# Kernel optimization log

Measured on AMD Instinct MI355X. Metric: run time of the kernel, lower is better.

## Reference

```python
import jax, jax.numpy as jnp
import numpy as np

B, T, C, H, HS = 4, 2048, 1024, 16, 64
EPS = 1e-5


def setup_inputs() -> dict:
    key = jax.random.key(0)
    ks = jax.random.split(key, 16)
    s = lambda k, shp, fan: jax.random.normal(k, shp, jnp.float32) * (fan ** -0.5)
    return {
        "x": jax.random.normal(ks[0], (B, T, C), jnp.float32),
        "wq": s(ks[1], (H, C, HS), C), "bq": jnp.zeros((H, HS), jnp.float32),
        "wk": s(ks[2], (H, C, HS), C), "bk": jnp.zeros((H, HS), jnp.float32),
        "wv": s(ks[3], (H, C, HS), C), "bv": jnp.zeros((H, HS), jnp.float32),
        "wp": s(ks[4], (C, C), C), "bp": jnp.zeros((C,), jnp.float32),
        "w1": s(ks[5], (C, 4 * C), C), "b1": jnp.zeros((4 * C,), jnp.float32),
        "w2": s(ks[6], (4 * C, C), 4 * C), "b2": jnp.zeros((C,), jnp.float32),
        "g1": jnp.ones((C,), jnp.float32), "be1": jnp.zeros((C,), jnp.float32),
        "g2": jnp.ones((C,), jnp.float32), "be2": jnp.zeros((C,), jnp.float32),
    }


def _layernorm(x, g, b):
    mu = jnp.mean(x, axis=-1, keepdims=True)
    var = jnp.mean(jnp.square(x - mu), axis=-1, keepdims=True)
    return (x - mu) * jax.lax.rsqrt(var + EPS) * g + b


def reference(x, wq, bq, wk, bk, wv, bv, wp, bp, w1, b1, w2, b2, g1, be1, g2, be2):
    Bc, Tc, Cc = x.shape
    h = _layernorm(x, g1, be1)
    # per-head projections stacked: [B,H,T,HS]
    q = jnp.einsum('btc,hcd->bhtd', h, wq) + bq[None, :, None, :]
    k = jnp.einsum('btc,hcd->bhtd', h, wk) + bk[None, :, None, :]
    v = jnp.einsum('btc,hcd->bhtd', h, wv) + bv[None, :, None, :]
    # NOTE: source scales by 1/sqrt(n_embd), not 1/sqrt(head_size)
    scores = jnp.einsum('bhtd,bhsd->bhts', q, k) * (Cc ** -0.5)
    causal = jnp.tril(jnp.ones((Tc, Tc), bool))
    scores = jnp.where(causal, scores, -jnp.inf)
    attn = jax.nn.softmax(scores, axis=-1)
    out = jnp.einsum('bhts,bhsd->bhtd', attn, v)
    out = out.transpose(0, 2, 1, 3).reshape(Bc, Tc, Cc)  # concat heads
    x = x + out @ wp + bp
    h2 = _layernorm(x, g2, be2)
    ffn = jax.nn.relu(h2 @ w1 + b1) @ w2 + b2
    return x + ffn
```

## Files before the change

kernel.cpp:

```cpp
#include <hip/hip_runtime.h>


constexpr int Bb = 4, Tt = 2048, Cc = 1024, Hh = 16, HSz = 64, Ff = 4096;
constexpr int Mrows = Bb * Tt;

typedef __attribute__((ext_vector_type(8))) short bf16x8;
typedef __attribute__((ext_vector_type(4))) float f32x4;

__device__ __forceinline__ ushort f2bf(float f) {
  uint u = __builtin_bit_cast(uint, f);
  uint r = (u + 0x7fffu + ((u >> 16) & 1u)) >> 16;
  return (ushort)r;
}
__device__ __forceinline__ float bf2f(ushort s) {
  return __builtin_bit_cast(float, ((uint)s) << 16);
}
__device__ __forceinline__ uint cvtpk_bf16(float lo, float hi) {
  uint r;
  asm("v_cvt_pk_bf16_f32 %0, %1, %2" : "=v"(r) : "v"(lo), "v"(hi));
  return r;
}
__device__ __forceinline__ void gload16(const void* g, void* l) {
  __builtin_amdgcn_global_load_lds(
      (const __attribute__((address_space(1))) void*)g,
      (__attribute__((address_space(3))) void*)l, 16, 0, 0);
}
#define VMCNT0 asm volatile("s_waitcnt vmcnt(0)" ::: "memory")
#define LGKM0                                          \
  do {                                                 \
    asm volatile("s_waitcnt lgkmcnt(0)" ::: "memory"); \
    __builtin_amdgcn_sched_barrier(0);                 \
  } while (0)
#define BARRIER __builtin_amdgcn_s_barrier()

__global__ __launch_bounds__(256) void ln_kernel(const float* __restrict__ x,
                                                 const float* __restrict__ g,
                                                 const float* __restrict__ b,
                                                 ushort* __restrict__ out) {
  int row = blockIdx.x;
  const float* xr = x + (size_t)row * Cc;
  int c4 = threadIdx.x * 4;
  float4 v = *(const float4*)(xr + c4);
  float s1 = v.x + v.y + v.z + v.w;
  float s2 = v.x * v.x + v.y * v.y + v.z * v.z + v.w * v.w;
#pragma unroll
  for (int off = 32; off >= 1; off >>= 1) {
    s1 += __shfl_xor(s1, off);
    s2 += __shfl_xor(s2, off);
  }
  __shared__ float red[8];
  int wid = threadIdx.x >> 6, lane = threadIdx.x & 63;
  if (lane == 0) { red[wid] = s1; red[4 + wid] = s2; }
  __syncthreads();
  float t1 = red[0] + red[1] + red[2] + red[3];
  float t2 = red[4] + red[5] + red[6] + red[7];
  float mu = t1 * (1.0f / Cc);
  float var = t2 * (1.0f / Cc) - mu * mu;
  float rs = rsqrtf(var + 1e-5f);
  float4 gv = *(const float4*)(g + c4);
  float4 bv = *(const float4*)(b + c4);
  ushort4 o;
  o.x = f2bf((v.x - mu) * rs * gv.x + bv.x);
  o.y = f2bf((v.y - mu) * rs * gv.y + bv.y);
  o.z = f2bf((v.z - mu) * rs * gv.z + bv.z);
  o.w = f2bf((v.w - mu) * rs * gv.w + bv.w);
  *(ushort4*)(out + (size_t)row * Cc + c4) = o;
}

__device__ __forceinline__ void tcast_body(const float* __restrict__ src,
                                           ushort* __restrict__ dst, int ldS,
                                           int ldD, int r0, int c0) {
  __shared__ float t[32][33];
  int c = threadIdx.x & 31, r8 = threadIdx.x >> 5;
#pragma unroll
  for (int i = 0; i < 4; ++i) {
    int r = r8 + i * 8;
    t[r][c] = src[(size_t)(r0 + r) * ldS + c0 + c];
  }
  __syncthreads();
#pragma unroll
  for (int i = 0; i < 4; ++i) {
    int rr = r8 + i * 8;
    dst[(size_t)(c0 + rr) * ldD + r0 + c] = f2bf(t[c][rr]);
  }
}

__global__ __launch_bounds__(256) void tcast_kernel(const float* __restrict__ src,
                                                    ushort* __restrict__ dst,
                                                    int ldS, int ldD) {
  tcast_body(src, dst, ldS, ldD, blockIdx.x * 32, blockIdx.y * 32);
}

__global__ __launch_bounds__(256) void tcast_qkv(const float* __restrict__ wq,
                                                 const float* __restrict__ wk,
                                                 const float* __restrict__ wv,
                                                 ushort* __restrict__ dst) {
  int z = blockIdx.z, zz = z >> 4, h = z & 15;
  const float* src = (zz == 0 ? wq : (zz == 1 ? wk : wv)) + (size_t)h * Cc * HSz;
  ushort* d = dst + (size_t)(zz * 1024 + h * 64) * 1024;
  tcast_body(src, d, HSz, Cc, blockIdx.x * 32, blockIdx.y * 32);
}

__global__ __launch_bounds__(256) void bias_concat(const float* __restrict__ bq,
                                                   const float* __restrict__ bk,
                                                   const float* __restrict__ bv,
                                                   float* __restrict__ dst) {
  int i = blockIdx.x * 256 + threadIdx.x;
  dst[i] = i < 1024 ? bq[i] : (i < 2048 ? bk[i - 1024] : bv[i - 2048]);
}

__device__ __forceinline__ void xcd_swz(int& bx, int& by) {
  int bid = blockIdx.x + blockIdx.y * gridDim.x;
  int cpx = (gridDim.x * gridDim.y) >> 3;
  int id = (bid & 7) * cpx + (bid >> 3);
  bx = id % gridDim.x;
  by = id / gridDim.x;
}

template <int MH, int NH>
__device__ __forceinline__ void mfma16(f32x4 (&acc)[8][4], bf16x8 (&a)[4][2],
                                       bf16x8 (&b)[2][2]) {
#pragma unroll
  for (int m = 0; m < 4; ++m)
#pragma unroll
    for (int n = 0; n < 2; ++n)
#pragma unroll
      for (int kk = 0; kk < 2; ++kk)
        acc[MH * 4 + m][NH * 2 + n] = __builtin_amdgcn_mfma_f32_16x16x32_bf16(
            a[m][kk], b[n][kk], acc[MH * 4 + m][NH * 2 + n], 0, 0, 0);
}

__device__ __forceinline__ void gemm256_main(const ushort* __restrict__ A,
                                             const ushort* __restrict__ Bt,
                                             int m0, int n0,
                                             ushort* __restrict__ As,
                                             ushort* __restrict__ Bs,
                                             f32x4 (&acc)[8][4]) {
  constexpr int NKT = 16;
  int tid = threadIdx.x, wid = tid >> 6, lane = tid & 63;
  int wr = wid >> 2, wc = wid & 3, fr = lane & 15, fq = lane >> 4;
  const ushort* Ag = A + (size_t)m0 * 1024;
  const ushort* Bg = Bt + (size_t)n0 * 1024;
  int r0 = tid >> 3, r1 = 64 + (tid >> 3);
  int sc = ((tid & 7) ^ ((tid >> 3) & 7)) << 3;

  auto stage = [&](int ktn, int h, int ns) {
    const ushort* g = (h < 2) ? Ag : Bg;
    ushort* l = ((h < 2) ? As : Bs) + ns * 16384 + (h & 1) * 8192;
    int kcol = ktn * 64, rbase = (h & 1) * 128;
    gload16(g + (size_t)(rbase + r0) * 1024 + kcol + sc, l + (size_t)wid * 512);
    gload16(g + (size_t)(rbase + r1) * 1024 + kcol + sc,
            l + (size_t)(512 + wid * 64) * 8);
  };
  auto readA = [&](int slot, int mh, bf16x8 (&a)[4][2]) {
#pragma unroll
    for (int m = 0; m < 4; ++m) {
      int row = wr * 128 + mh * 64 + m * 16 + fr;
#pragma unroll
      for (int kk = 0; kk < 2; ++kk)
        a[m][kk] = *(const bf16x8*)&As[slot * 16384 + row * 64 +
                                       (((kk * 4 + fq) ^ (row & 7)) << 3)];
    }
  };
  auto readB = [&](int slot, int nh, bf16x8 (&b)[2][2]) {
#pragma unroll
    for (int n = 0; n < 2; ++n) {
      int row = wc * 64 + nh * 32 + n * 16 + fr;
#pragma unroll
      for (int kk = 0; kk < 2; ++kk)
        b[n][kk] = *(const bf16x8*)&Bs[slot * 16384 + row * 64 +
                                       (((kk * 4 + fq) ^ (row & 7)) << 3)];
    }
  };

  stage(0, 0, 0); stage(0, 1, 0); stage(0, 2, 0); stage(0, 3, 0);
  VMCNT0;
  BARRIER;

  bf16x8 a[4][2], b0[2][2], b1[2][2];
#pragma unroll 1
  for (int kt = 0; kt < NKT; ++kt) {
    int slot = kt & 1, ns = slot ^ 1;
    bool st = (kt + 1 < NKT);
    readA(slot, 0, a);
    readB(slot, 0, b0);
    if (st) { stage(kt + 1, 0, ns); stage(kt + 1, 2, ns); }
    BARRIER;
    LGKM0;
    __builtin_amdgcn_s_setprio(1);
    mfma16<0, 0>(acc, a, b0);
    __builtin_amdgcn_s_setprio(0);
    BARRIER;
    readB(slot, 1, b1);
    if (st) { stage(kt + 1, 1, ns); stage(kt + 1, 3, ns); }
    BARRIER;
    LGKM0;
    __builtin_amdgcn_s_setprio(1);
    mfma16<0, 1>(acc, a, b1);
    __builtin_amdgcn_s_setprio(0);
    BARRIER;
    readA(slot, 1, a);
    BARRIER;
    LGKM0;
    __builtin_amdgcn_s_setprio(1);
    mfma16<1, 0>(acc, a, b0);
    __builtin_amdgcn_s_setprio(0);
    BARRIER;
    __builtin_amdgcn_s_setprio(1);
    mfma16<1, 1>(acc, a, b1);
    __builtin_amdgcn_s_setprio(0);
    VMCNT0;
    BARRIER;
  }
}

__global__ __launch_bounds__(512, 2) void gemm256_relu(
    const ushort* __restrict__ A, const ushort* __restrict__ Bt,
    const float* __restrict__ bias, ushort* __restrict__ Cout, int ldc) {
  __shared__ __align__(16) ushort As[2 * 256 * 64];
  __shared__ __align__(16) ushort Bs[2 * 256 * 64];
  f32x4 acc[8][4] = {};
  int bx, by;
  xcd_swz(bx, by);
  int m0 = by * 256, n0 = bx * 256;
  gemm256_main(A, Bt, m0, n0, As, Bs, acc);
  int lane = threadIdx.x & 63, wid = threadIdx.x >> 6;
  int wr = wid >> 2, wc = wid & 3, fr = lane & 15, fq = lane >> 4;
#pragma unroll
  for (int i = 0; i < 8; ++i) {
    int gm = m0 + wr * 128 + (i >> 2) * 64 + (i & 3) * 16 + fq * 4;
#pragma unroll
    for (int j2 = 0; j2 < 4; ++j2) {
      int gn = n0 + wc * 64 + (j2 >> 1) * 32 + (j2 & 1) * 16 + fr;
      float bsv = bias[gn];
#pragma unroll
      for (int j = 0; j < 4; ++j)
        Cout[(size_t)(gm + j) * ldc + gn] = f2bf(fmaxf(acc[i][j2][j] + bsv, 0.f));
    }
  }
}

__global__ __launch_bounds__(512, 2) void gemm256_ffn2(
    const ushort* __restrict__ A, int lda, const ushort* __restrict__ Bt,
    int ldb, const float* __restrict__ bias, const float* __restrict__ res,
    float* __restrict__ Cout, int ldc, int K) {
  __shared__ __align__(16) ushort As[2 * 256 * 64];
  __shared__ __align__(16) ushort Bs[2 * 128 * 64];
  f32x4 acc[8][2] = {};
  int bx, by;
  xcd_swz(bx, by);
  int m0 = by * 256, n0 = bx * 128;
  int tid = threadIdx.x, wid = tid >> 6, lane = tid & 63;
  int wr = wid >> 2, wc = wid & 3, fr = lane & 15, fq = lane >> 4;
  const ushort* Ag = A + (size_t)m0 * lda;
  const ushort* Bg = Bt + (size_t)n0 * ldb;
  int r0 = tid >> 3, r1 = 64 + (tid >> 3);
  int sc = ((tid & 7) ^ ((tid >> 3) & 7)) << 3;
  int NKT = K >> 6;

  auto stageA = [&](int ktn, int h, int ns) {
    ushort* l = As + ns * 16384 + h * 8192;
    int kcol = ktn * 64, rbase = h * 128;
    gload16(Ag + (size_t)(rbase + r0) * lda + kcol + sc, l + (size_t)wid * 512);
    gload16(Ag + (size_t)(rbase + r1) * lda + kcol + sc,
            l + (size_t)(512 + wid * 64) * 8);
  };
  auto stageB = [&](int ktn, int h, int ns) {
    ushort* l = Bs + ns * 8192 + h * 4096;
    int kcol = ktn * 64, rbase = h * 64;
    gload16(Bg + (size_t)(rbase + r0) * ldb + kcol + sc, l + (size_t)wid * 512);
  };
  auto readA = [&](int slot, int mh, bf16x8 (&a)[4][2]) {
#pragma unroll
    for (int m = 0; m < 4; ++m) {
      int row = wr * 128 + mh * 64 + m * 16 + fr;
#pragma unroll
      for (int kk = 0; kk < 2; ++kk)
        a[m][kk] = *(const bf16x8*)&As[slot * 16384 + row * 64 +
                                       (((kk * 4 + fq) ^ (row & 7)) << 3)];
    }
  };
  auto readB = [&](int slot, int nh, bf16x8 (&b)[2]) {
    int row = wc * 32 + nh * 16 + fr;
#pragma unroll
    for (int kk = 0; kk < 2; ++kk)
      b[kk] = *(const bf16x8*)&Bs[slot * 8192 + row * 64 +
                                  (((kk * 4 + fq) ^ (row & 7)) << 3)];
  };
  auto mfma8 = [&](int mh, int nh, bf16x8 (&a)[4][2], bf16x8 (&b)[2]) {
#pragma unroll
    for (int m = 0; m < 4; ++m)
#pragma unroll
      for (int kk = 0; kk < 2; ++kk)
        acc[mh * 4 + m][nh] = __builtin_amdgcn_mfma_f32_16x16x32_bf16(
            a[m][kk], b[kk], acc[mh * 4 + m][nh], 0, 0, 0);
  };

  stageA(0, 0, 0); stageA(0, 1, 0); stageB(0, 0, 0); stageB(0, 1, 0);
  VMCNT0;
  BARRIER;

  bf16x8 a[4][2], b0[2], b1[2];
#pragma unroll 1
  for (int kt = 0; kt < NKT; ++kt) {
    int slot = kt & 1, ns = slot ^ 1;
    bool st = (kt + 1 < NKT);
    readA(slot, 0, a);
    readB(slot, 0, b0);
    if (st) { stageA(kt + 1, 0, ns); stageB(kt + 1, 0, ns); }
    BARRIER;
    LGKM0;
    __builtin_amdgcn_s_setprio(1);
    mfma8(0, 0, a, b0);
    __builtin_amdgcn_s_setprio(0);
    BARRIER;
    readB(slot, 1, b1);
    if (st) { stageA(kt + 1, 1, ns); stageB(kt + 1, 1, ns); }
    BARRIER;
    LGKM0;
    __builtin_amdgcn_s_setprio(1);
    mfma8(0, 1, a, b1);
    __builtin_amdgcn_s_setprio(0);
    BARRIER;
    readA(slot, 1, a);
    BARRIER;
    LGKM0;
    __builtin_amdgcn_s_setprio(1);
    mfma8(1, 0, a, b0);
    __builtin_amdgcn_s_setprio(0);
    BARRIER;
    __builtin_amdgcn_s_setprio(1);
    mfma8(1, 1, a, b1);
    __builtin_amdgcn_s_setprio(0);
    VMCNT0;
    BARRIER;
  }

#pragma unroll
  for (int i = 0; i < 8; ++i) {
    int gm = m0 + wr * 128 + (i >> 2) * 64 + (i & 3) * 16 + fq * 4;
#pragma unroll
    for (int nh = 0; nh < 2; ++nh) {
      int gn = n0 + wc * 32 + nh * 16 + fr;
      float bsv = bias[gn];
#pragma unroll
      for (int j = 0; j < 4; ++j) {
        int row = gm + j;
        Cout[(size_t)row * ldc + gn] =
            acc[i][nh][j] + bsv + res[(size_t)row * ldc + gn];
      }
    }
  }
}

__device__ __forceinline__ void gemm_main(const ushort* __restrict__ A, int lda,
                                          const ushort* __restrict__ Bt, int ldb,
                                          int K, int m0, int n0,
                                          ushort* __restrict__ As,
                                          ushort* __restrict__ Bs,
                                          f32x4 (&acc)[4][2]) {
  int tid = threadIdx.x, wid = tid >> 6, lane = tid & 63;
  int wr = wid >> 2, wc = wid & 3, fr = lane & 15, fq = lane >> 4;
  const ushort* Ag = A + (size_t)m0 * lda;
  const ushort* Bg = Bt + (size_t)n0 * ldb;
  for (int k0 = 0; k0 < K; k0 += 64) {
#pragma unroll
    for (int c = 0; c < 2; ++c) {
      int slot = c * 512 + tid;
      int row = slot >> 3, s = slot & 7;
      int sw = (s << 3) ^ ((row & 7) << 3);
      gload16(Ag + (size_t)row * lda + k0 + sw, As + (size_t)(c * 512 + wid * 64) * 8);
      gload16(Bg + (size_t)row * ldb + k0 + sw, Bs + (size_t)(c * 512 + wid * 64) * 8);
    }
    __syncthreads();
    bf16x8 av[4][2], bv[2][2];
#pragma unroll
    for (int m = 0; m < 4; ++m) {
      int row = wr * 64 + m * 16 + fr;
#pragma unroll
      for (int ks = 0; ks < 2; ++ks)
        av[m][ks] = *(const bf16x8*)&As[row * 64 + (((ks * 4 + fq) ^ (row & 7)) << 3)];
    }
#pragma unroll
    for (int n = 0; n < 2; ++n) {
      int row = wc * 32 + n * 16 + fr;
#pragma unroll
      for (int ks = 0; ks < 2; ++ks)
        bv[n][ks] = *(const bf16x8*)&Bs[row * 64 + (((ks * 4 + fq) ^ (row & 7)) << 3)];
    }
#pragma unroll
    for (int m = 0; m < 4; ++m)
#pragma unroll
      for (int n = 0; n < 2; ++n)
#pragma unroll
        for (int ks = 0; ks < 2; ++ks)
          acc[m][n] = __builtin_amdgcn_mfma_f32_16x16x32_bf16(
              av[m][ks], bv[n][ks], acc[m][n], 0, 0, 0);
    __syncthreads();
  }
}

template <bool RELU, bool HASRES, bool OUTBF16>
__global__ __launch_bounds__(512) void gemm_bf16(
    const ushort* __restrict__ A, int lda, const ushort* __restrict__ Bt,
    int ldb, const float* __restrict__ bias, const float* __restrict__ res,
    void* __restrict__ Cout, int ldc, int K) {
  __shared__ __align__(16) ushort As[128 * 64];
  __shared__ __align__(16) ushort Bs[128 * 64];
  f32x4 acc[4][2] = {};
  int bx, by;
  xcd_swz(bx, by);
  int m0 = by * 128, n0 = bx * 128;
  gemm_main(A, lda, Bt, ldb, K, m0, n0, As, Bs, acc);
  int lane = threadIdx.x & 63, wid = threadIdx.x >> 6;
  int wr = wid >> 2, wc = wid & 3, fr = lane & 15, fq = lane >> 4;
#pragma unroll
  for (int m = 0; m < 4; ++m) {
    int gm = m0 + wr * 64 + m * 16 + fq * 4;
#pragma unroll
    for (int n = 0; n < 2; ++n) {
      int gn = n0 + wc * 32 + n * 16 + fr;
      float bsv = bias[gn];
#pragma unroll
      for (int j = 0; j < 4; ++j) {
        int row = gm + j;
        float v = acc[m][n][j] + bsv;
        if constexpr (HASRES) v += res[(size_t)row * ldc + gn];
        if constexpr (RELU) v = fmaxf(v, 0.f);
        if constexpr (OUTBF16)
          ((ushort*)Cout)[(size_t)row * ldc + gn] = f2bf(v);
        else
          ((float*)Cout)[(size_t)row * ldc + gn] = v;
      }
    }
  }
}

__global__ __launch_bounds__(512) void gemm_qkv(const ushort* __restrict__ A,
                                                const ushort* __restrict__ Bt,
                                                const float* __restrict__ bias,
                                                ushort* __restrict__ q,
                                                ushort* __restrict__ k,
                                                ushort* __restrict__ vt) {
  __shared__ __align__(16) ushort As[128 * 64];
  __shared__ __align__(16) ushort Bs[128 * 64];
  f32x4 acc[4][2] = {};
  int bx, by;
  xcd_swz(bx, by);
  int m0 = by * 128, n0 = bx * 128;
  gemm_main(A, 1024, Bt, 1024, 1024, m0, n0, As, Bs, acc);
  int lane = threadIdx.x & 63, wid = threadIdx.x >> 6;
  int wr = wid >> 2, wc = wid & 3, fr = lane & 15, fq = lane >> 4;
  const float qscale = 1.4426950408889634f / 32.0f;
#pragma unroll
  for (int m = 0; m < 4; ++m) {
    int gm = m0 + wr * 64 + m * 16 + fq * 4;
#pragma unroll
    for (int n = 0; n < 2; ++n) {
      int gn = n0 + wc * 32 + n * 16 + fr;
      float bsv = bias[gn];
      if (gn < 1024) {
#pragma unroll
        for (int j = 0; j < 4; ++j)
          q[(size_t)(gm + j) * 1024 + gn] = f2bf((acc[m][n][j] + bsv) * qscale);
      } else if (gn < 2048) {
        int col = gn - 1024;
#pragma unroll
        for (int j = 0; j < 4; ++j)
          k[(size_t)(gm + j) * 1024 + col] = f2bf(acc[m][n][j] + bsv);
      } else {
        int dd = gn - 2048, h = dd >> 6, d = dd & 63;
        int bbr = gm >> 11, t = gm & 2047;
        ushort4 pw = {f2bf(acc[m][n][0] + bsv), f2bf(acc[m][n][1] + bsv),
                      f2bf(acc[m][n][2] + bsv), f2bf(acc[m][n][3] + bsv)};
        *(ushort4*)&vt[(((size_t)(bbr * 16 + h)) * 64 + d) * 2048 + t] = pw;
      }
    }
  }
}

constexpr int QB = 128, KVB = 64;
__global__ __launch_bounds__(512) void attn_kernel(const ushort* __restrict__ Qb,
                                                   const ushort* __restrict__ Kb,
                                                   const ushort* __restrict__ Vt,
                                                   ushort* __restrict__ att) {
  __shared__ __align__(16) ushort Klds[2][64 * 64];
  __shared__ __align__(16) ushort Vlds[2][64 * 64];
  __shared__ __align__(16) ushort Plds[8][16 * 64];
  int tid = threadIdx.x, wid = tid >> 6, lane = tid & 63;
  int fr = lane & 15, fq = lane >> 4;
  int bh = blockIdx.y, bb = bh >> 4, hh = bh & 15;
  const ushort* qkbase = Qb + ((size_t)bb * Tt) * Cc + hh * HSz;
  const ushort* Kbase = Kb + ((size_t)bb * Tt) * Cc + hh * HSz;
  const ushort* Vbase = Vt + ((size_t)(bb * Hh + hh)) * HSz * Tt;
  int srow = tid >> 3;
  int ssw = ((tid & 7) << 3) ^ ((srow & 7) << 3);

#pragma unroll 1
  for (int pass = 0; pass < 2; ++pass) {
    int qt = pass ? (Tt / QB - 1 - (int)blockIdx.x) : (int)blockIdx.x;
    int q0 = qt * QB;
    int q0w = q0 + wid * 16;

    bf16x8 Qreg[2];
#pragma unroll
    for (int d2 = 0; d2 < 2; ++d2)
      Qreg[d2] = *(const bf16x8*)(qkbase + (size_t)(q0w + fr) * Cc + d2 * 32 + fq * 8);
    f32x4 Oa[4] = {};
    float mrow = -1e30f, lrow = 0.f;
    int nt = q0 / KVB + 2;

    __syncthreads();
    gload16(Kbase + (size_t)srow * Cc + ssw, (char*)Klds[0] + wid * 1024);
    gload16(Vbase + (size_t)srow * Tt + ssw, (char*)Vlds[0] + wid * 1024);

#pragma unroll 1
    for (int kt = 0; kt < nt; ++kt) {
      int t0 = kt * KVB;
      int c = kt & 1;
      __syncthreads();
      if (kt + 1 < nt) {
        int t0n = t0 + KVB;
        gload16(Kbase + (size_t)(t0n + srow) * Cc + ssw,
                (char*)Klds[c ^ 1] + wid * 1024);
        gload16(Vbase + (size_t)srow * Tt + t0n + ssw,
                (char*)Vlds[c ^ 1] + wid * 1024);
      }
      if (q0w + 15 < t0) continue;

      const char* Kc = (const char*)Klds[c];
      const char* Vc = (const char*)Vlds[c];
      bf16x8 kf[4][2];
#pragma unroll
      for (int ks = 0; ks < 4; ++ks)
#pragma unroll
        for (int d2 = 0; d2 < 2; ++d2) {
          int row = ks * 16 + fr;
          int off = (d2 * 64 + fq * 16) ^ ((row & 7) << 4);
          kf[ks][d2] = *(const bf16x8*)(Kc + row * 128 + off);
        }
      f32x4 accs[4] = {};
      __builtin_amdgcn_s_setprio(1);
#pragma unroll
      for (int ks = 0; ks < 4; ++ks) {
        accs[ks] = __builtin_amdgcn_mfma_f32_16x16x32_bf16(
            kf[ks][0], Qreg[0], accs[ks], 0, 0, 0);
        accs[ks] = __builtin_amdgcn_mfma_f32_16x16x32_bf16(
            kf[ks][1], Qreg[1], accs[ks], 0, 0, 0);
      }
      __builtin_amdgcn_s_setprio(0);

      float sv[4][4];
      float vmax = -1e30f;
      if (t0 + 63 <= q0w) {
#pragma unroll
        for (int ks = 0; ks < 4; ++ks)
#pragma unroll
          for (int j = 0; j < 4; ++j) {
            sv[ks][j] = accs[ks][j];
            vmax = fmaxf(vmax, sv[ks][j]);
          }
      } else {
        int qg = q0w + fr;
#pragma unroll
        for (int ks = 0; ks < 4; ++ks)
#pragma unroll
          for (int j = 0; j < 4; ++j) {
            int kg = t0 + ks * 16 + fq * 4 + j;
            float s = accs[ks][j];
            s = (kg <= qg) ? s : -1e30f;
            sv[ks][j] = s;
            vmax = fmaxf(vmax, s);
          }
      }
      float mnew = mrow;
      if (!__all(vmax <= mrow + 11.0f)) {
        float rmax = fmaxf(vmax, __shfl_xor(vmax, 16));
        rmax = fmaxf(rmax, __shfl_xor(rmax, 32));
        mnew = fmaxf(mrow, rmax);
        float sf = exp2f(mrow - mnew);
        mrow = mnew;
        lrow *= sf;
#pragma unroll
        for (int j = 0; j < 4; ++j) {
          float sfo = __shfl(sf, fq * 4 + j);
#pragma unroll
          for (int ds = 0; ds < 4; ++ds) Oa[ds][j] *= sfo;
        }
      }
      char* pbase = (char*)Plds[wid] + fr * 128;
#pragma unroll
      for (int ks = 0; ks < 4; ++ks) {
        float p0 = exp2f(sv[ks][0] - mnew);
        float p1 = exp2f(sv[ks][1] - mnew);
        float p2 = exp2f(sv[ks][2] - mnew);
        float p3 = exp2f(sv[ks][3] - mnew);
        lrow += (p0 + p1) + (p2 + p3);
        uint2 pw = {cvtpk_bf16(p0, p1), cvtpk_bf16(p2, p3)};
        int off = (ks * 32 + fq * 8) ^ ((fr & 7) << 4);
        *(uint2*)(pbase + off) = pw;
      }

      bf16x8 vf[4][2];
#pragma unroll
      for (int ds = 0; ds < 4; ++ds)
#pragma unroll
        for (int k2 = 0; k2 < 2; ++k2) {
          int row = ds * 16 + fr;
          int off = (k2 * 64 + fq * 16) ^ ((row & 7) << 4);
          vf[ds][k2] = *(const bf16x8*)(Vc + row * 128 + off);
        }
      bf16x8 pf[2];
#pragma unroll
      for (int k2 = 0; k2 < 2; ++k2) {
        int off = (k2 * 64 + fq * 16) ^ ((fr & 7) << 4);
        pf[k2] = *(const bf16x8*)((const char*)Plds[wid] + fr * 128 + off);
      }
      __builtin_amdgcn_s_setprio(1);
#pragma unroll
      for (int ds = 0; ds < 4; ++ds) {
        Oa[ds] = __builtin_amdgcn_mfma_f32_16x16x32_bf16(
            pf[0], vf[ds][0], Oa[ds], 0, 0, 0);
        Oa[ds] = __builtin_amdgcn_mfma_f32_16x16x32_bf16(
            pf[1], vf[ds][1], Oa[ds], 0, 0, 0);
      }
      __builtin_amdgcn_s_setprio(0);
    }

    {
      lrow += __shfl_xor(lrow, 16);
      lrow += __shfl_xor(lrow, 32);
      float linv = 1.f / lrow;
#pragma unroll
      for (int j = 0; j < 4; ++j) {
        float lo = __shfl(linv, fq * 4 + j);
        int qg = q0w + fq * 4 + j;
        ushort* orow = att + (size_t)(bb * Tt + qg) * Cc + hh * HSz;
#pragma unroll
        for (int ds = 0; ds < 4; ++ds)
          orow[ds * 16 + fr] = f2bf(Oa[ds][j] * lo);
      }
    }
  }
}

extern "C" void kernel_launch(void* const* d_in, const int* in_sizes, int n_in,
                              void* d_out, int out_size, void* d_ws,
                              size_t ws_size, hipStream_t stream) {
  const float* x = (const float*)d_in[0];
  const float* wq = (const float*)d_in[1];
  const float* bq = (const float*)d_in[2];
  const float* wk = (const float*)d_in[3];
  const float* bk = (const float*)d_in[4];
  const float* wv = (const float*)d_in[5];
  const float* bv = (const float*)d_in[6];
  const float* wp = (const float*)d_in[7];
  const float* bp = (const float*)d_in[8];
  const float* w1 = (const float*)d_in[9];
  const float* b1 = (const float*)d_in[10];
  const float* w2 = (const float*)d_in[11];
  const float* b2 = (const float*)d_in[12];
  const float* g1 = (const float*)d_in[13];
  const float* be1 = (const float*)d_in[14];
  const float* g2 = (const float*)d_in[15];
  const float* be2 = (const float*)d_in[16];
  float* out = (float*)d_out;

  ushort* Qb = (ushort*)d_ws;
  ushort* Kb = Qb + (size_t)8388608;
  ushort* Vt = Kb + (size_t)8388608;
  ushort* att = Vt + (size_t)8388608;
  ushort* ffh = Qb;
  ushort* h1b = att + (size_t)8388608;
  float* x2 = (float*)(h1b + (size_t)8388608);
  ushort* wqkvT = (ushort*)(x2 + (size_t)8388608);
  ushort* wpT = wqkvT + (size_t)3145728;
  ushort* w1T = wpT + (size_t)1048576;
  ushort* w2T = w1T + (size_t)4194304;
  float* bqkv = (float*)(w2T + (size_t)4194304);

  tcast_qkv<<<dim3(32, 2, 48), 256, 0, stream>>>(wq, wk, wv, wqkvT);
  tcast_kernel<<<dim3(32, 32), 256, 0, stream>>>(wp, wpT, 1024, 1024);
  tcast_kernel<<<dim3(32, 128), 256, 0, stream>>>(w1, w1T, 4096, 1024);
  tcast_kernel<<<dim3(128, 32), 256, 0, stream>>>(w2, w2T, 1024, 4096);
  bias_concat<<<dim3(12), 256, 0, stream>>>(bq, bk, bv, bqkv);

  ln_kernel<<<dim3(Mrows), 256, 0, stream>>>(x, g1, be1, h1b);
  gemm_qkv<<<dim3(24, 64), 512, 0, stream>>>(h1b, wqkvT, bqkv, Qb, Kb, Vt);
  attn_kernel<<<dim3(Tt / QB / 2, Bb * Hh), 512, 0, stream>>>(Qb, Kb, Vt, att);
  gemm_bf16<false, true, false><<<dim3(8, 64), 512, 0, stream>>>(
      att, 1024, wpT, 1024, bp, x, x2, 1024, 1024);
  ln_kernel<<<dim3(Mrows), 256, 0, stream>>>(x2, g2, be2, h1b);
  gemm256_relu<<<dim3(16, 32), 512, 0, stream>>>(h1b, w1T, b1, ffh, 4096);
  gemm256_ffn2<<<dim3(8, 32), 512, 0, stream>>>(
      ffh, 4096, w2T, 4096, b2, x2, out, 1024, 4096);
}
```

Measured before the change: 364.8 us.

## Load both A halves up front and merge MFMA phases in projection GEMM

Restructures the K-loop of this GEMM kernel (bias plus residual epilogue) so both A fragment halves are read from LDS at the start. All next-tile global-to-LDS staging is issued at once, and the four 8-MFMA phases collapse into two 16-MFMA phases. The aim is fewer barriers and waits per K step and longer uninterrupted MFMA runs. In exchange it holds more A fragment registers, which may lower occupancy, and it issues all staging in one burst instead of interleaving it with compute.

```diff
diff --git a/kernel.cpp b/kernel.cpp
--- a/kernel.cpp
+++ b/kernel.cpp
@@ -287,50 +287,49 @@
       b[kk] = *(const bf16x8*)&Bs[slot * 8192 + row * 64 +
                                   (((kk * 4 + fq) ^ (row & 7)) << 3)];
   };
-  auto mfma8 = [&](int mh, int nh, bf16x8 (&a)[4][2], bf16x8 (&b)[2]) {
+  auto mfma16n = [&](int nh, bf16x8 (&a0)[4][2], bf16x8 (&a1)[4][2],
+                     bf16x8 (&b)[2]) {
 #pragma unroll
     for (int m = 0; m < 4; ++m)
 #pragma unroll
       for (int kk = 0; kk < 2; ++kk)
-        acc[mh * 4 + m][nh] = __builtin_amdgcn_mfma_f32_16x16x32_bf16(
-            a[m][kk], b[kk], acc[mh * 4 + m][nh], 0, 0, 0);
+        acc[m][nh] = __builtin_amdgcn_mfma_f32_16x16x32_bf16(
+            a0[m][kk], b[kk], acc[m][nh], 0, 0, 0);
+#pragma unroll
+    for (int m = 0; m < 4; ++m)
+#pragma unroll
+      for (int kk = 0; kk < 2; ++kk)
+        acc[4 + m][nh] = __builtin_amdgcn_mfma_f32_16x16x32_bf16(
+            a1[m][kk], b[kk], acc[4 + m][nh], 0, 0, 0);
   };
 
   stageA(0, 0, 0); stageA(0, 1, 0); stageB(0, 0, 0); stageB(0, 1, 0);
   VMCNT0;
   BARRIER;
 
-  bf16x8 a[4][2], b0[2], b1[2];
+  bf16x8 a0[4][2], a1[4][2], b0[2], b1[2];
 #pragma unroll 1
   for (int kt = 0; kt < NKT; ++kt) {
     int slot = kt & 1, ns = slot ^ 1;
     bool st = (kt + 1 < NKT);
-    readA(slot, 0, a);
+    readA(slot, 0, a0);
+    readA(slot, 1, a1);
     readB(slot, 0, b0);
-    if (st) { stageA(kt + 1, 0, ns); stageB(kt + 1, 0, ns); }
+    if (st) {
+      stageA(kt + 1, 0, ns); stageA(kt + 1, 1, ns);
+      stageB(kt + 1, 0, ns); stageB(kt + 1, 1, ns);
+    }
     BARRIER;
     LGKM0;
     __builtin_amdgcn_s_setprio(1);
-    mfma8(0, 0, a, b0);
+    mfma16n(0, a0, a1, b0);
     __builtin_amdgcn_s_setprio(0);
     BARRIER;
     readB(slot, 1, b1);
-    if (st) { stageA(kt + 1, 1, ns); stageB(kt + 1, 1, ns); }
     BARRIER;
     LGKM0;
     __builtin_amdgcn_s_setprio(1);
-    mfma8(0, 1, a, b1);
-    __builtin_amdgcn_s_setprio(0);
-    BARRIER;
-    readA(slot, 1, a);
-    BARRIER;
-    LGKM0;
-    __builtin_amdgcn_s_setprio(1);
-    mfma8(1, 0, a, b0);
-    __builtin_amdgcn_s_setprio(0);
-    BARRIER;
-    __builtin_amdgcn_s_setprio(1);
-    mfma8(1, 1, a, b1);
+    mfma16n(1, a0, a1, b1);
     __builtin_amdgcn_s_setprio(0);
     VMCNT0;
     BARRIER;
```

New measurement: 359.2 us. No clear change (-1.5%).
